# Performance work log

Measured on AMD Instinct MI355X. Metric: run time of the kernel, lower is better.

Reference implementation:

```python
import jax, jax.numpy as jnp
import numpy as np

D_MODEL = 1024
HEAD_SIZE = 64
BLOCK_SIZE = 2048
B, T = 4, 2048


def setup_inputs() -> dict:
    key = jax.random.key(0)
    ks = jax.random.split(key, 7)
    s = 1.0 / np.sqrt(D_MODEL)
    x = jax.random.normal(ks[0], (B, T, D_MODEL), dtype=jnp.float32)
    Wq = jax.random.uniform(ks[1], (D_MODEL, HEAD_SIZE), jnp.float32, -s, s)
    bq = jax.random.uniform(ks[2], (HEAD_SIZE,), jnp.float32, -s, s)
    Wk = jax.random.uniform(ks[3], (D_MODEL, HEAD_SIZE), jnp.float32, -s, s)
    bk = jax.random.uniform(ks[4], (HEAD_SIZE,), jnp.float32, -s, s)
    Wv = jax.random.uniform(ks[5], (D_MODEL, HEAD_SIZE), jnp.float32, -s, s)
    return {"x": x, "Wq": Wq, "bq": bq, "Wk": Wk, "bk": bk, "Wv": Wv, "mask": 1}


def reference(x, Wq, bq, Wk, bk, Wv, mask):
    # x: [B, T, C]; single attention head, dropout is identity (eval/p=0)
    Tlen = x.shape[1]
    q = x @ Wq + bq              # [B, T, hs]
    k = x @ Wk + bk              # [B, T, hs]
    v = x @ Wv                   # [B, T, hs] (no bias)
    hs = k.shape[-1]
    # Faithful to source: weights = QK^T / hs**(-0.5)  ==  QK^T * sqrt(hs)
    w = jnp.einsum('btd,bsd->bts', q, k) * jnp.sqrt(jnp.asarray(hs, x.dtype))
    if mask:
        causal = jnp.tril(jnp.ones((Tlen, Tlen), dtype=bool))
        w = jnp.where(causal, w, jnp.asarray(-jnp.inf, w.dtype))
    w = jax.nn.softmax(w, axis=-1)
    out = jnp.einsum('bts,bsd->btd', w, v)  # [B, T, hs]
    return out
```

## Files before the change

### kernel.cpp

```cpp
#include <hip/hip_runtime.h>
#include <hip/hip_bf16.h>

#define D_MODEL 1024
#define HS 64
#define T_LEN 2048
#define JCH 256
#define NCH 8

typedef __attribute__((ext_vector_type(8))) short bf16x8;
typedef __attribute__((ext_vector_type(4))) float f32x4;

__device__ inline void split8(const float* v, int4& hi, int4& lo) {
    union { unsigned short u[8]; int4 v4; } uh, ul;
    #pragma unroll
    for (int i = 0; i < 8; ++i) {
        const unsigned int b = __float_as_uint(v[i]);
        const unsigned short h = (unsigned short)(b >> 16);
        const float r = v[i] - __uint_as_float((unsigned int)h << 16);
        uh.u[i] = h;
        ul.u[i] = (unsigned short)(__float_as_uint(r) >> 16);
    }
    hi = uh.v4; lo = ul.v4;
}

__device__ inline unsigned short f2bf_rne(float f) {
    const unsigned int b = __float_as_uint(f);
    return (unsigned short)((b + 0x7FFFu + ((b >> 16) & 1u)) >> 16);
}
__device__ inline float bf2f(unsigned short h) {
    return __uint_as_float((unsigned int)h << 16);
}

__device__ inline void async_copy16(const short* g, short* l) {
    __builtin_amdgcn_global_load_lds(
        (const __attribute__((address_space(1))) void*)g,
        (__attribute__((address_space(3))) void*)l, 16, 0, 0);
}

__global__ __launch_bounds__(256) void prep_kernel(
    const float* __restrict__ Wq, const float* __restrict__ Wk,
    const float* __restrict__ Wv,
    short* __restrict__ wh, short* __restrict__ wl)
{
    __shared__ float tile[64][69];
    const int tid = threadIdx.x;
    const int wb  = blockIdx.x;
    const int kb  = wb & 15;
    const int m   = wb >> 4;
    const float* W = (m == 0) ? Wq : (m == 1) ? Wk : Wv;
    #pragma unroll
    for (int it = 0; it < 4; ++it) {
        const int idx = tid + 256 * it;
        const int kr = idx >> 4, c4 = idx & 15;
        *(float4*)&tile[kr][4 * c4] =
            *(const float4*)(W + (size_t)(kb * 64 + kr) * HS + 4 * c4);
    }
    __syncthreads();
    #pragma unroll
    for (int i = 0; i < 2; ++i) {
        const int s    = tid + 256 * i;
        const int ntl  = s >> 7;
        const int kcl  = (s >> 6) & 1;
        const int lane = s & 63;
        const int n    = ntl * 16 + (lane & 15);
        const int krel = kcl * 32 + (lane >> 4) * 8;
        float v[8];
        #pragma unroll
        for (int e = 0; e < 8; ++e) v[e] = tile[krel + e][n];
        int4 hi, lo;
        split8(v, hi, lo);
        const size_t off =
            ((size_t)((m * 4 + ntl) * 32 + kb * 2 + kcl) * 64 + lane) * 8;
        *(int4*)(wh + off) = hi;
        *(int4*)(wl + off) = lo;
    }
}

__device__ inline void stage_B(const short* __restrict__ wh,
                               const short* __restrict__ wl,
                               short* Bdst, int ch, int wave, int lane) {
    #pragma unroll
    for (int ii = 0; ii < 12; ++ii) {
        const int g   = wave * 12 + ii;
        const int nt  = g >> 2;
        const int kcl = (g >> 1) & 1;
        const int p   = g & 1;
        const short* src = (p ? wl : wh)
                         + ((size_t)(nt * 32 + ch * 2 + kcl)) * 512;
        async_copy16(src + lane * 8, Bdst + g * 512);
    }
}

__global__ __launch_bounds__(256) void qkv_kernel(
    const float* __restrict__ x,
    const short* __restrict__ wh, const short* __restrict__ wl,
    const float* __restrict__ bq, const float* __restrict__ bk,
    short* __restrict__ qfh, short* __restrict__ qfl,
    short* __restrict__ kfh, short* __restrict__ kfl, short* __restrict__ vf)
{
    __shared__ __align__(16) short A_lds[2][8 * 512];
    __shared__ __align__(16) short B_lds[2][48 * 512];

    const int tid   = threadIdx.x;
    const int r0    = blockIdx.x * 32;
    const int wave  = tid >> 6;
    const int lane  = tid & 63;
    const int mt_l  = tid >> 7;
    const int kcl_l = (tid >> 6) & 1;
    const int nt0   = wave * 3;

    const float* xrow = x + (size_t)(r0 + mt_l * 16 + (lane & 15)) * D_MODEL
                          + kcl_l * 32 + (lane >> 4) * 8;

    f32x4 acc[2][3];
    #pragma unroll
    for (int mt = 0; mt < 2; ++mt)
        #pragma unroll
        for (int j = 0; j < 3; ++j) acc[mt][j] = (f32x4)(0.f);

    {
        stage_B(wh, wl, &B_lds[0][0], 0, wave, lane);
        float v[8];
        *(float4*)&v[0] = *(const float4*)(xrow);
        *(float4*)&v[4] = *(const float4*)(xrow + 4);
        int4 hi, lo;
        split8(v, hi, lo);
        *(int4*)&A_lds[0][(mt_l * 4 + kcl_l * 2 + 0) * 512 + lane * 8] = hi;
        *(int4*)&A_lds[0][(mt_l * 4 + kcl_l * 2 + 1) * 512 + lane * 8] = lo;
    }
    __syncthreads();

    int cur = 0;
    for (int t = 0; t < 16; ++t) {
        float v[8];
        const bool pf = (t < 15);
        if (pf) {
            *(float4*)&v[0] = *(const float4*)(xrow + (t + 1) * 64);
            *(float4*)&v[4] = *(const float4*)(xrow + (t + 1) * 64 + 4);
            stage_B(wh, wl, &B_lds[cur ^ 1][0], t + 1, wave, lane);
        }
        #pragma unroll
        for (int kcl = 0; kcl < 2; ++kcl) {
            const bf16x8 a0h = *(const bf16x8*)&A_lds[cur][(0 + kcl * 2 + 0) * 512 + lane * 8];
            const bf16x8 a0l = *(const bf16x8*)&A_lds[cur][(0 + kcl * 2 + 1) * 512 + lane * 8];
            const bf16x8 a1h = *(const bf16x8*)&A_lds[cur][(4 + kcl * 2 + 0) * 512 + lane * 8];
            const bf16x8 a1l = *(const bf16x8*)&A_lds[cur][(4 + kcl * 2 + 1) * 512 + lane * 8];
            #pragma unroll
            for (int j = 0; j < 3; ++j) {
                const int gb = (nt0 + j) * 4 + kcl * 2;
                const bf16x8 bh = *(const bf16x8*)&B_lds[cur][(gb + 0) * 512 + lane * 8];
                const bf16x8 bl = *(const bf16x8*)&B_lds[cur][(gb + 1) * 512 + lane * 8];
                acc[0][j] = __builtin_amdgcn_mfma_f32_16x16x32_bf16(a0h, bh, acc[0][j], 0, 0, 0);
                acc[0][j] = __builtin_amdgcn_mfma_f32_16x16x32_bf16(a0h, bl, acc[0][j], 0, 0, 0);
                acc[0][j] = __builtin_amdgcn_mfma_f32_16x16x32_bf16(a0l, bh, acc[0][j], 0, 0, 0);
                acc[1][j] = __builtin_amdgcn_mfma_f32_16x16x32_bf16(a1h, bh, acc[1][j], 0, 0, 0);
                acc[1][j] = __builtin_amdgcn_mfma_f32_16x16x32_bf16(a1h, bl, acc[1][j], 0, 0, 0);
                acc[1][j] = __builtin_amdgcn_mfma_f32_16x16x32_bf16(a1l, bh, acc[1][j], 0, 0, 0);
            }
        }
        if (pf) {
            int4 hi, lo;
            split8(v, hi, lo);
            *(int4*)&A_lds[cur ^ 1][(mt_l * 4 + kcl_l * 2 + 0) * 512 + lane * 8] = hi;
            *(int4*)&A_lds[cur ^ 1][(mt_l * 4 + kcl_l * 2 + 1) * 512 + lane * 8] = lo;
        }
        __syncthreads();
        cur ^= 1;
    }

    const int quad = lane >> 4;
    const int l15  = lane & 15;
    #pragma unroll
    for (int mt = 0; mt < 2; ++mt) {
        const int rowb = r0 + mt * 16 + quad * 4;
        #pragma unroll
        for (int j = 0; j < 3; ++j) {
            const f32x4 a = acc[mt][j];
            const int c = (nt0 + j) * 16 + l15;
            if (c < 128) {
                const int cc    = (c < 64) ? c : (c - 64);
                const float bias = (c < 64) ? bq[cc] : bk[cc];
                short* dsth = (c < 64) ? qfh : kfh;
                short* dstl = (c < 64) ? qfl : kfl;
                const int tile16 = rowb >> 4;
                const int kc2   = cc >> 5;
                const int quadd = (cc & 31) >> 3;
                const int e     = cc & 7;
                #pragma unroll
                for (int r = 0; r < 4; ++r) {
                    const float val = a[r] + bias;
                    const unsigned int b = __float_as_uint(val);
                    const unsigned short h = (unsigned short)(b >> 16);
                    const float res = val - __uint_as_float((unsigned int)h << 16);
                    const unsigned short l16 = (unsigned short)(__float_as_uint(res) >> 16);
                    const int laned = ((rowb + r) & 15) | (quadd << 4);
                    const size_t off = ((size_t)((tile16 * 2 + kc2) * 64 + laned)) * 8 + e;
                    dsth[off] = (short)h;
                    dstl[off] = (short)l16;
                }
            } else {
                const int cv    = c - 128;
                const int vb    = rowb >> 6;
                const int jc2   = (rowb & 63) >> 5;
                const int quadd = (rowb & 31) >> 3;
                const int gg    = jc2 * 4 + (cv >> 4);
                const int laned = (cv & 15) | (quadd << 4);
                const size_t base = ((size_t)((vb * 8 + gg) * 64 + laned)) * 8 + (rowb & 7);
                short4 pk;
                pk.x = (short)f2bf_rne(a[0]);
                pk.y = (short)f2bf_rne(a[1]);
                pk.z = (short)f2bf_rne(a[2]);
                pk.w = (short)f2bf_rne(a[3]);
                *(short4*)(vf + base) = pk;
            }
        }
    }
}

__global__ __launch_bounds__(256) void attn_kernel(
    const short* __restrict__ qfh, const short* __restrict__ qfl,
    const short* __restrict__ kfh, const short* __restrict__ kfl,
    const short* __restrict__ vf, const int* __restrict__ maskp,
    float* __restrict__ part_O, float* __restrict__ part_ml, int BT)
{
    __shared__ __align__(16) short Kh[4096], Kl[4096];
    __shared__ __align__(16) short Vt[4096];
    __shared__ __align__(16) short Pl[4][16 * 72];

    const int tile  = blockIdx.x;
    const int chunk = blockIdx.y;
    const int r0 = tile * 64;
    const int tb = r0 / T_LEN;
    const int t0 = r0 - tb * T_LEN;
    const int mask = (*maskp != 0);
    const int n_max = mask ? (t0 + 64) : T_LEN;
    const int j0 = chunk * JCH;
    if (j0 >= n_max) return;
    const int hi_j = min(j0 + JCH, n_max);
    const int njt = (hi_j - j0 + 63) >> 6;

    const int tid  = threadIdx.x;
    const int w    = tid >> 6;
    const int lane = tid & 63;
    const int quad = lane >> 4;
    const int l15  = lane & 15;
    const int rw0  = t0 + 16 * w;
    const int rowa = r0 + 16 * w + quad * 4;

    bf16x8 qh[2], ql[2];
    {
        const size_t qt = (size_t)(r0 >> 4) + w;
        #pragma unroll
        for (int kc = 0; kc < 2; ++kc) {
            qh[kc] = *(const bf16x8*)&qfh[((qt * 2 + kc) * 64 + lane) * 8];
            ql[kc] = *(const bf16x8*)&qfl[((qt * 2 + kc) * 64 + lane) * 8];
        }
    }

    f32x4 oacc[4];
    #pragma unroll
    for (int nt = 0; nt < 4; ++nt) oacc[nt] = (f32x4)(0.f);
    float m_r[4] = {-INFINITY, -INFINITY, -INFINITY, -INFINITY};
    float l_r[4] = {0.f, 0.f, 0.f, 0.f};

    for (int jt = 0; jt < njt; ++jt) {
        const int jbase = j0 + jt * 64;
        __syncthreads();
        {
            const size_t kt0 = (size_t)(tb * 128) + (jbase >> 4);
            const size_t vb  = (size_t)(tb * 32) + (jbase >> 6);
            #pragma unroll
            for (int ii = 0; ii < 6; ++ii) {
                const int g = w * 6 + ii;
                if (g < 8) {
                    const short* src = kfh + ((kt0 + (g >> 1)) * 2 + (g & 1)) * 512;
                    async_copy16(src + lane * 8, &Kh[g * 512]);
                } else if (g < 16) {
                    const int gg = g - 8;
                    const short* src = kfl + ((kt0 + (gg >> 1)) * 2 + (gg & 1)) * 512;
                    async_copy16(src + lane * 8, &Kl[gg * 512]);
                } else {
                    const int gg = g - 16;
                    const short* src = vf + (vb * 8 + gg) * 512;
                    async_copy16(src + lane * 8, &Vt[gg * 512]);
                }
            }
        }
        __syncthreads();

        const bool active = (!mask) || (jbase <= rw0 + 15);
        if (active) {
            f32x4 sacc[4];
            #pragma unroll
            for (int jsub = 0; jsub < 4; ++jsub) {
                f32x4 s = (f32x4)(0.f);
                #pragma unroll
                for (int kc = 0; kc < 2; ++kc) {
                    const bf16x8 kh = *(const bf16x8*)&Kh[((jsub * 2 + kc) * 64 + lane) * 8];
                    const bf16x8 kl = *(const bf16x8*)&Kl[((jsub * 2 + kc) * 64 + lane) * 8];
                    s = __builtin_amdgcn_mfma_f32_16x16x32_bf16(qh[kc], kh, s, 0, 0, 0);
                    s = __builtin_amdgcn_mfma_f32_16x16x32_bf16(qh[kc], kl, s, 0, 0, 0);
                    s = __builtin_amdgcn_mfma_f32_16x16x32_bf16(ql[kc], kh, s, 0, 0, 0);
                }
                sacc[jsub] = s;
            }
            float sval[4][4], rmax[4];
            #pragma unroll
            for (int r = 0; r < 4; ++r) rmax[r] = -INFINITY;
            #pragma unroll
            for (int jsub = 0; jsub < 4; ++jsub) {
                const int jg = jbase + jsub * 16 + l15;
                #pragma unroll
                for (int r = 0; r < 4; ++r) {
                    const int tg = rw0 + quad * 4 + r;
                    const float vv = (mask && (jg > tg)) ? -INFINITY : 8.0f * sacc[jsub][r];
                    sval[jsub][r] = vv;
                    rmax[r] = fmaxf(rmax[r], vv);
                }
            }
            #pragma unroll
            for (int d = 1; d < 16; d <<= 1)
                #pragma unroll
                for (int r = 0; r < 4; ++r)
                    rmax[r] = fmaxf(rmax[r], __shfl_xor(rmax[r], d));
            float alpha[4], msafe[4];
            #pragma unroll
            for (int r = 0; r < 4; ++r) {
                const float mn = fmaxf(m_r[r], rmax[r]);
                msafe[r] = (mn == -INFINITY) ? 0.f : mn;
                alpha[r] = __expf(m_r[r] - msafe[r]);
                m_r[r] = mn;
            }
            short* Pw = &Pl[w][0];
            float rsum[4] = {0.f, 0.f, 0.f, 0.f};
            #pragma unroll
            for (int jsub = 0; jsub < 4; ++jsub) {
                #pragma unroll
                for (int r = 0; r < 4; ++r) {
                    const float e = __expf(sval[jsub][r] - msafe[r]);
                    const unsigned short eb = f2bf_rne(e);
                    Pw[(quad * 4 + r) * 72 + jsub * 16 + l15] = (short)eb;
                    rsum[r] += bf2f(eb);
                }
            }
            #pragma unroll
            for (int d = 1; d < 16; d <<= 1)
                #pragma unroll
                for (int r = 0; r < 4; ++r)
                    rsum[r] += __shfl_xor(rsum[r], d);
            #pragma unroll
            for (int r = 0; r < 4; ++r)
                l_r[r] = l_r[r] * alpha[r] + rsum[r];
            #pragma unroll
            for (int nt = 0; nt < 4; ++nt)
                #pragma unroll
                for (int r = 0; r < 4; ++r)
                    oacc[nt][r] *= alpha[r];
            bf16x8 pf[2];
            #pragma unroll
            for (int jc = 0; jc < 2; ++jc)
                pf[jc] = *(const bf16x8*)&Pw[l15 * 72 + jc * 32 + quad * 8];
            #pragma unroll
            for (int nt = 0; nt < 4; ++nt) {
                #pragma unroll
                for (int jc = 0; jc < 2; ++jc) {
                    const bf16x8 vfr = *(const bf16x8*)&Vt[((jc * 4 + nt) * 64 + lane) * 8];
                    oacc[nt] = __builtin_amdgcn_mfma_f32_16x16x32_bf16(pf[jc], vfr, oacc[nt], 0, 0, 0);
                }
            }
        }
    }

    #pragma unroll
    for (int nt = 0; nt < 4; ++nt)
        #pragma unroll
        for (int r = 0; r < 4; ++r)
            part_O[((size_t)(rowa + r) * NCH + chunk) * HS + nt * 16 + l15] = oacc[nt][r];
    if (l15 == 0) {
        #pragma unroll
        for (int r = 0; r < 4; ++r) {
            float2 ml;
            ml.x = m_r[r];
            ml.y = l_r[r];
            *(float2*)(part_ml + ((size_t)(rowa + r) * NCH + chunk) * 2) = ml;
        }
    }
}

__global__ __launch_bounds__(256) void combine_kernel(
    const float* __restrict__ part_O, const float* __restrict__ part_ml,
    const int* __restrict__ maskp, float* __restrict__ out)
{
    const int f = blockIdx.x * 256 + threadIdx.x;
    const int row = f >> 4;
    const int d4 = (f & 15) * 4;
    const int t = row & (T_LEN - 1);
    const int mask = (*maskp != 0);
    const int n = mask ? (t + 1) : T_LEN;
    const int nc = (n + JCH - 1) / JCH;

    const float2* mlp = (const float2*)(part_ml + (size_t)row * NCH * 2);
    float M = -INFINITY;
    for (int c = 0; c < nc; ++c) M = fmaxf(M, mlp[c].x);
    float L = 0.f;
    float Ox = 0.f, Oy = 0.f, Oz = 0.f, Ow = 0.f;
    for (int c = 0; c < nc; ++c) {
        const float2 ml = mlp[c];
        const float w = __expf(ml.x - M);
        L += ml.y * w;
        const float4 p = *(const float4*)(part_O + ((size_t)row * NCH + c) * HS + d4);
        Ox = fmaf(p.x, w, Ox);
        Oy = fmaf(p.y, w, Oy);
        Oz = fmaf(p.z, w, Oz);
        Ow = fmaf(p.w, w, Ow);
    }
    float4 res;
    res.x = Ox / L;
    res.y = Oy / L;
    res.z = Oz / L;
    res.w = Ow / L;
    *(float4*)(out + (size_t)row * HS + d4) = res;
}

extern "C" void kernel_launch(void* const* d_in, const int* in_sizes, int n_in,
                              void* d_out, int out_size, void* d_ws, size_t ws_size,
                              hipStream_t stream) {
    const float* x  = (const float*)d_in[0];
    const float* Wq = (const float*)d_in[1];
    const float* bq = (const float*)d_in[2];
    const float* Wk = (const float*)d_in[3];
    const float* bk = (const float*)d_in[4];
    const float* Wv = (const float*)d_in[5];
    const int* maskp = (const int*)d_in[6];

    const int BT = in_sizes[0] / D_MODEL;

    float* pO  = (float*)d_ws;
    float* pml = pO + (size_t)BT * NCH * HS;
    short* wh  = (short*)(pml + (size_t)BT * NCH * 2);
    short* wl  = wh + (size_t)192 * D_MODEL;
    short* qfh = wl + (size_t)192 * D_MODEL;
    short* qfl = qfh + (size_t)BT * HS;
    short* kfh = qfl + (size_t)BT * HS;
    short* kfl = kfh + (size_t)BT * HS;
    short* vf  = kfl + (size_t)BT * HS;

    prep_kernel<<<48, 256, 0, stream>>>(Wq, Wk, Wv, wh, wl);
    qkv_kernel<<<BT / 32, 256, 0, stream>>>(x, wh, wl, bq, bk,
                                            qfh, qfl, kfh, kfl, vf);
    dim3 agrid(BT / 64, NCH);
    attn_kernel<<<agrid, 256, 0, stream>>>(qfh, qfl, kfh, kfl, vf, maskp,
                                           pO, pml, BT);
    combine_kernel<<<(BT * 16) / 256, 256, 0, stream>>>(pO, pml, maskp, (float*)d_out);
}
```

Baseline: 138.8 us.

## Fuse four kernels into one persistent kernel with grid barriers

Replaces the prep, QKV projection, attention and combine launches with a single persistent kernel of 256 blocks that loops over work items in each phase. Phases are separated by a software grid barrier built on an atomic counter. The aim is to remove per-launch overhead and the idle tails between kernels. In exchange it relies on all 256 blocks being co-resident, which a 112KB shared buffer and one block per CU make plausible. It also caps parallelism in each phase at 256 blocks and adds barrier spin cost.

```diff
diff --git a/kernel.cpp b/kernel.cpp
--- a/kernel.cpp
+++ b/kernel.cpp
@@ -6,6 +6,7 @@
 #define T_LEN 2048
 #define JCH 256
 #define NCH 8
+#define NBLK 256
 
 typedef __attribute__((ext_vector_type(8))) short bf16x8;
 typedef __attribute__((ext_vector_type(4))) float f32x4;
@@ -35,45 +36,6 @@
     __builtin_amdgcn_global_load_lds(
         (const __attribute__((address_space(1))) void*)g,
         (__attribute__((address_space(3))) void*)l, 16, 0, 0);
-}
-
-__global__ __launch_bounds__(256) void prep_kernel(
-    const float* __restrict__ Wq, const float* __restrict__ Wk,
-    const float* __restrict__ Wv,
-    short* __restrict__ wh, short* __restrict__ wl)
-{
-    __shared__ float tile[64][69];
-    const int tid = threadIdx.x;
-    const int wb  = blockIdx.x;
-    const int kb  = wb & 15;
-    const int m   = wb >> 4;
-    const float* W = (m == 0) ? Wq : (m == 1) ? Wk : Wv;
-    #pragma unroll
-    for (int it = 0; it < 4; ++it) {
-        const int idx = tid + 256 * it;
-        const int kr = idx >> 4, c4 = idx & 15;
-        *(float4*)&tile[kr][4 * c4] =
-            *(const float4*)(W + (size_t)(kb * 64 + kr) * HS + 4 * c4);
-    }
-    __syncthreads();
-    #pragma unroll
-    for (int i = 0; i < 2; ++i) {
-        const int s    = tid + 256 * i;
-        const int ntl  = s >> 7;
-        const int kcl  = (s >> 6) & 1;
-        const int lane = s & 63;
-        const int n    = ntl * 16 + (lane & 15);
-        const int krel = kcl * 32 + (lane >> 4) * 8;
-        float v[8];
-        #pragma unroll
-        for (int e = 0; e < 8; ++e) v[e] = tile[krel + e][n];
-        int4 hi, lo;
-        split8(v, hi, lo);
-        const size_t off =
-            ((size_t)((m * 4 + ntl) * 32 + kb * 2 + kcl) * 64 + lane) * 8;
-        *(int4*)(wh + off) = hi;
-        *(int4*)(wl + off) = lo;
-    }
 }
 
 __device__ inline void stage_B(const short* __restrict__ wh,
@@ -91,335 +53,399 @@
     }
 }
 
-__global__ __launch_bounds__(256) void qkv_kernel(
+__device__ unsigned int g_tick;
+
+__device__ __forceinline__ void grid_barrier() {
+    __syncthreads();
+    __threadfence();
+    if (threadIdx.x == 0) {
+        const unsigned int t = __hip_atomic_fetch_add(
+            &g_tick, 1u, __ATOMIC_ACQ_REL, __HIP_MEMORY_SCOPE_AGENT);
+        const unsigned int target = ((t >> 8) + 1u) << 8;
+        while (__hip_atomic_load(&g_tick, __ATOMIC_ACQUIRE,
+                                 __HIP_MEMORY_SCOPE_AGENT) < target) {
+            __builtin_amdgcn_s_sleep(2);
+        }
+    }
+    __syncthreads();
+    __threadfence();
+}
+
+__global__ __launch_bounds__(256, 1) void fused_kernel(
     const float* __restrict__ x,
-    const short* __restrict__ wh, const short* __restrict__ wl,
+    const float* __restrict__ Wq, const float* __restrict__ Wk,
+    const float* __restrict__ Wv,
     const float* __restrict__ bq, const float* __restrict__ bk,
+    const int* __restrict__ maskp,
+    short* __restrict__ wh, short* __restrict__ wl,
     short* __restrict__ qfh, short* __restrict__ qfl,
-    short* __restrict__ kfh, short* __restrict__ kfl, short* __restrict__ vf)
+    short* __restrict__ kfh, short* __restrict__ kfl, short* __restrict__ vf,
+    float* __restrict__ part_O, float* __restrict__ part_ml,
+    float* __restrict__ out, int BT)
 {
-    __shared__ __align__(16) short A_lds[2][8 * 512];
-    __shared__ __align__(16) short B_lds[2][48 * 512];
-
-    const int tid   = threadIdx.x;
-    const int r0    = blockIdx.x * 32;
-    const int wave  = tid >> 6;
-    const int lane  = tid & 63;
-    const int mt_l  = tid >> 7;
-    const int kcl_l = (tid >> 6) & 1;
-    const int nt0   = wave * 3;
-
-    const float* xrow = x + (size_t)(r0 + mt_l * 16 + (lane & 15)) * D_MODEL
-                          + kcl_l * 32 + (lane >> 4) * 8;
-
-    f32x4 acc[2][3];
-    #pragma unroll
-    for (int mt = 0; mt < 2; ++mt)
+    __shared__ __align__(16) char smem[114688];
+    const int tid = threadIdx.x;
+    const int bx  = blockIdx.x;
+
+    if (bx < 48) {
+        float (*tile)[69] = (float (*)[69])smem;
+        const int kb = bx & 15;
+        const int m  = bx >> 4;
+        const float* W = (m == 0) ? Wq : (m == 1) ? Wk : Wv;
         #pragma unroll
-        for (int j = 0; j < 3; ++j) acc[mt][j] = (f32x4)(0.f);
-
-    {
-        stage_B(wh, wl, &B_lds[0][0], 0, wave, lane);
-        float v[8];
-        *(float4*)&v[0] = *(const float4*)(xrow);
-        *(float4*)&v[4] = *(const float4*)(xrow + 4);
-        int4 hi, lo;
-        split8(v, hi, lo);
-        *(int4*)&A_lds[0][(mt_l * 4 + kcl_l * 2 + 0) * 512 + lane * 8] = hi;
-        *(int4*)&A_lds[0][(mt_l * 4 + kcl_l * 2 + 1) * 512 + lane * 8] = lo;
-    }
-    __syncthreads();
-
-    int cur = 0;
-    for (int t = 0; t < 16; ++t) {
-        float v[8];
-        const bool pf = (t < 15);
-        if (pf) {
-            *(float4*)&v[0] = *(const float4*)(xrow + (t + 1) * 64);
-            *(float4*)&v[4] = *(const float4*)(xrow + (t + 1) * 64 + 4);
-            stage_B(wh, wl, &B_lds[cur ^ 1][0], t + 1, wave, lane);
-        }
+        for (int it = 0; it < 4; ++it) {
+            const int idx = tid + 256 * it;
+            const int kr = idx >> 4, c4 = idx & 15;
+            *(float4*)&tile[kr][4 * c4] =
+                *(const float4*)(W + (size_t)(kb * 64 + kr) * HS + 4 * c4);
+        }
+        __syncthreads();
         #pragma unroll
-        for (int kcl = 0; kcl < 2; ++kcl) {
-            const bf16x8 a0h = *(const bf16x8*)&A_lds[cur][(0 + kcl * 2 + 0) * 512 + lane * 8];
-            const bf16x8 a0l = *(const bf16x8*)&A_lds[cur][(0 + kcl * 2 + 1) * 512 + lane * 8];
-            const bf16x8 a1h = *(const bf16x8*)&A_lds[cur][(4 + kcl * 2 + 0) * 512 + lane * 8];
-            const bf16x8 a1l = *(const bf16x8*)&A_lds[cur][(4 + kcl * 2 + 1) * 512 + lane * 8];
-            #pragma unroll
-            for (int j = 0; j < 3; ++j) {
-                const int gb = (nt0 + j) * 4 + kcl * 2;
-                const bf16x8 bh = *(const bf16x8*)&B_lds[cur][(gb + 0) * 512 + lane * 8];
-                const bf16x8 bl = *(const bf16x8*)&B_lds[cur][(gb + 1) * 512 + lane * 8];
-                acc[0][j] = __builtin_amdgcn_mfma_f32_16x16x32_bf16(a0h, bh, acc[0][j], 0, 0, 0);
-                acc[0][j] = __builtin_amdgcn_mfma_f32_16x16x32_bf16(a0h, bl, acc[0][j], 0, 0, 0);
-                acc[0][j] = __builtin_amdgcn_mfma_f32_16x16x32_bf16(a0l, bh, acc[0][j], 0, 0, 0);
-                acc[1][j] = __builtin_amdgcn_mfma_f32_16x16x32_bf16(a1h, bh, acc[1][j], 0, 0, 0);
-                acc[1][j] = __builtin_amdgcn_mfma_f32_16x16x32_bf16(a1h, bl, acc[1][j], 0, 0, 0);
-                acc[1][j] = __builtin_amdgcn_mfma_f32_16x16x32_bf16(a1l, bh, acc[1][j], 0, 0, 0);
-            }
-        }
-        if (pf) {
+        for (int i = 0; i < 2; ++i) {
+            const int s    = tid + 256 * i;
+            const int ntl  = s >> 7;
+            const int kcl  = (s >> 6) & 1;
+            const int lane = s & 63;
+            const int n    = ntl * 16 + (lane & 15);
+            const int krel = kcl * 32 + (lane >> 4) * 8;
+            float v[8];
+            #pragma unroll
+            for (int e = 0; e < 8; ++e) v[e] = tile[krel + e][n];
             int4 hi, lo;
             split8(v, hi, lo);
-            *(int4*)&A_lds[cur ^ 1][(mt_l * 4 + kcl_l * 2 + 0) * 512 + lane * 8] = hi;
-            *(int4*)&A_lds[cur ^ 1][(mt_l * 4 + kcl_l * 2 + 1) * 512 + lane * 8] = lo;
+            const size_t off =
+                ((size_t)((m * 4 + ntl) * 32 + kb * 2 + kcl) * 64 + lane) * 8;
+            *(int4*)(wh + off) = hi;
+            *(int4*)(wl + off) = lo;
+        }
+    }
+    grid_barrier();
+
+    for (int g = bx; g < (BT >> 5); g += NBLK) {
+        short* const Abase = (short*)smem;
+        short* const Bbase = (short*)(smem + 16384);
+        const int r0    = g * 32;
+        const int wave  = tid >> 6;
+        const int lane  = tid & 63;
+        const int mt_l  = tid >> 7;
+        const int kcl_l = (tid >> 6) & 1;
+        const int nt0   = wave * 3;
+
+        const float* xrow = x + (size_t)(r0 + mt_l * 16 + (lane & 15)) * D_MODEL
+                              + kcl_l * 32 + (lane >> 4) * 8;
+
+        f32x4 acc[2][3];
+        #pragma unroll
+        for (int mt = 0; mt < 2; ++mt)
+            #pragma unroll
+            for (int j = 0; j < 3; ++j) acc[mt][j] = (f32x4)(0.f);
+
+        {
+            stage_B(wh, wl, Bbase, 0, wave, lane);
+            float v[8];
+            *(float4*)&v[0] = *(const float4*)(xrow);
+            *(float4*)&v[4] = *(const float4*)(xrow + 4);
+            int4 hi, lo;
+            split8(v, hi, lo);
+            *(int4*)&Abase[(mt_l * 4 + kcl_l * 2 + 0) * 512 + lane * 8] = hi;
+            *(int4*)&Abase[(mt_l * 4 + kcl_l * 2 + 1) * 512 + lane * 8] = lo;
         }
         __syncthreads();
-        cur ^= 1;
-    }
-
-    const int quad = lane >> 4;
-    const int l15  = lane & 15;
-    #pragma unroll
-    for (int mt = 0; mt < 2; ++mt) {
-        const int rowb = r0 + mt * 16 + quad * 4;
+
+        int cur = 0;
+        for (int t = 0; t < 16; ++t) {
+            float v[8];
+            const bool pf = (t < 15);
+            if (pf) {
+                *(float4*)&v[0] = *(const float4*)(xrow + (t + 1) * 64);
+                *(float4*)&v[4] = *(const float4*)(xrow + (t + 1) * 64 + 4);
+                stage_B(wh, wl, Bbase + (cur ^ 1) * 24576, t + 1, wave, lane);
+            }
+            const short* Ac = Abase + cur * 4096;
+            const short* Bc = Bbase + cur * 24576;
+            #pragma unroll
+            for (int kcl = 0; kcl < 2; ++kcl) {
+                const bf16x8 a0h = *(const bf16x8*)&Ac[(0 + kcl * 2 + 0) * 512 + lane * 8];
+                const bf16x8 a0l = *(const bf16x8*)&Ac[(0 + kcl * 2 + 1) * 512 + lane * 8];
+                const bf16x8 a1h = *(const bf16x8*)&Ac[(4 + kcl * 2 + 0) * 512 + lane * 8];
+                const bf16x8 a1l = *(const bf16x8*)&Ac[(4 + kcl * 2 + 1) * 512 + lane * 8];
+                #pragma unroll
+                for (int j = 0; j < 3; ++j) {
+                    const int gb = (nt0 + j) * 4 + kcl * 2;
+                    const bf16x8 bh = *(const bf16x8*)&Bc[(gb + 0) * 512 + lane * 8];
+                    const bf16x8 bl = *(const bf16x8*)&Bc[(gb + 1) * 512 + lane * 8];
+                    acc[0][j] = __builtin_amdgcn_mfma_f32_16x16x32_bf16(a0h, bh, acc[0][j], 0, 0, 0);
+                    acc[0][j] = __builtin_amdgcn_mfma_f32_16x16x32_bf16(a0h, bl, acc[0][j], 0, 0, 0);
+                    acc[0][j] = __builtin_amdgcn_mfma_f32_16x16x32_bf16(a0l, bh, acc[0][j], 0, 0, 0);
+                    acc[1][j] = __builtin_amdgcn_mfma_f32_16x16x32_bf16(a1h, bh, acc[1][j], 0, 0, 0);
+                    acc[1][j] = __builtin_amdgcn_mfma_f32_16x16x32_bf16(a1h, bl, acc[1][j], 0, 0, 0);
+                    acc[1][j] = __builtin_amdgcn_mfma_f32_16x16x32_bf16(a1l, bh, acc[1][j], 0, 0, 0);
+                }
+            }
+            if (pf) {
+                int4 hi, lo;
+                split8(v, hi, lo);
+                short* An = Abase + (cur ^ 1) * 4096;
+                *(int4*)&An[(mt_l * 4 + kcl_l * 2 + 0) * 512 + lane * 8] = hi;
+                *(int4*)&An[(mt_l * 4 + kcl_l * 2 + 1) * 512 + lane * 8] = lo;
+            }
+            __syncthreads();
+            cur ^= 1;
+        }
+
+        const int quad = lane >> 4;
+        const int l15  = lane & 15;
         #pragma unroll
-        for (int j = 0; j < 3; ++j) {
-            const f32x4 a = acc[mt][j];
-            const int c = (nt0 + j) * 16 + l15;
-            if (c < 128) {
-                const int cc    = (c < 64) ? c : (c - 64);
-                const float bias = (c < 64) ? bq[cc] : bk[cc];
-                short* dsth = (c < 64) ? qfh : kfh;
-                short* dstl = (c < 64) ? qfl : kfl;
-                const int tile16 = rowb >> 4;
-                const int kc2   = cc >> 5;
-                const int quadd = (cc & 31) >> 3;
-                const int e     = cc & 7;
-                #pragma unroll
-                for (int r = 0; r < 4; ++r) {
-                    const float val = a[r] + bias;
-                    const unsigned int b = __float_as_uint(val);
-                    const unsigned short h = (unsigned short)(b >> 16);
-                    const float res = val - __uint_as_float((unsigned int)h << 16);
-                    const unsigned short l16 = (unsigned short)(__float_as_uint(res) >> 16);
-                    const int laned = ((rowb + r) & 15) | (quadd << 4);
-                    const size_t off = ((size_t)((tile16 * 2 + kc2) * 64 + laned)) * 8 + e;
-                    dsth[off] = (short)h;
-                    dstl[off] = (short)l16;
-                }
-            } else {
-                const int cv    = c - 128;
-                const int vb    = rowb >> 6;
-                const int jc2   = (rowb & 63) >> 5;
-                const int quadd = (rowb & 31) >> 3;
-                const int gg    = jc2 * 4 + (cv >> 4);
-                const int laned = (cv & 15) | (quadd << 4);
-                const size_t base = ((size_t)((vb * 8 + gg) * 64 + laned)) * 8 + (rowb & 7);
-                short4 pk;
-                pk.x = (short)f2bf_rne(a[0]);
-                pk.y = (short)f2bf_rne(a[1]);
-                pk.z = (short)f2bf_rne(a[2]);
-                pk.w = (short)f2bf_rne(a[3]);
-                *(short4*)(vf + base) = pk;
-            }
-        }
-    }
-}
-
-__global__ __launch_bounds__(256) void attn_kernel(
-    const short* __restrict__ qfh, const short* __restrict__ qfl,
-    const short* __restrict__ kfh, const short* __restrict__ kfl,
-    const short* __restrict__ vf, const int* __restrict__ maskp,
-    float* __restrict__ part_O, float* __restrict__ part_ml, int BT)
-{
-    __shared__ __align__(16) short Kh[4096], Kl[4096];
-    __shared__ __align__(16) short Vt[4096];
-    __shared__ __align__(16) short Pl[4][16 * 72];
-
-    const int tile  = blockIdx.x;
-    const int chunk = blockIdx.y;
-    const int r0 = tile * 64;
-    const int tb = r0 / T_LEN;
-    const int t0 = r0 - tb * T_LEN;
-    const int mask = (*maskp != 0);
-    const int n_max = mask ? (t0 + 64) : T_LEN;
-    const int j0 = chunk * JCH;
-    if (j0 >= n_max) return;
-    const int hi_j = min(j0 + JCH, n_max);
-    const int njt = (hi_j - j0 + 63) >> 6;
-
-    const int tid  = threadIdx.x;
-    const int w    = tid >> 6;
-    const int lane = tid & 63;
-    const int quad = lane >> 4;
-    const int l15  = lane & 15;
-    const int rw0  = t0 + 16 * w;
-    const int rowa = r0 + 16 * w + quad * 4;
-
-    bf16x8 qh[2], ql[2];
+        for (int mt = 0; mt < 2; ++mt) {
+            const int rowb = r0 + mt * 16 + quad * 4;
+            #pragma unroll
+            for (int j = 0; j < 3; ++j) {
+                const f32x4 a = acc[mt][j];
+                const int c = (nt0 + j) * 16 + l15;
+                if (c < 128) {
+                    const int cc    = (c < 64) ? c : (c - 64);
+                    const float bias = (c < 64) ? bq[cc] : bk[cc];
+                    short* dsth = (c < 64) ? qfh : kfh;
+                    short* dstl = (c < 64) ? qfl : kfl;
+                    const int tile16 = rowb >> 4;
+                    const int kc2   = cc >> 5;
+                    const int quadd = (cc & 31) >> 3;
+                    const int e     = cc & 7;
+                    #pragma unroll
+                    for (int r = 0; r < 4; ++r) {
+                        const float val = a[r] + bias;
+                        const unsigned int b = __float_as_uint(val);
+                        const unsigned short h = (unsigned short)(b >> 16);
+                        const float res = val - __uint_as_float((unsigned int)h << 16);
+                        const unsigned short l16 = (unsigned short)(__float_as_uint(res) >> 16);
+                        const int laned = ((rowb + r) & 15) | (quadd << 4);
+                        const size_t off = ((size_t)((tile16 * 2 + kc2) * 64 + laned)) * 8 + e;
+                        dsth[off] = (short)h;
+                        dstl[off] = (short)l16;
+                    }
+                } else {
+                    const int cv    = c - 128;
+                    const int vb    = rowb >> 6;
+                    const int jc2   = (rowb & 63) >> 5;
+                    const int quadd = (rowb & 31) >> 3;
+                    const int gg    = jc2 * 4 + (cv >> 4);
+                    const int laned = (cv & 15) | (quadd << 4);
+                    const size_t base = ((size_t)((vb * 8 + gg) * 64 + laned)) * 8 + (rowb & 7);
+                    short4 pk;
+                    pk.x = (short)f2bf_rne(a[0]);
+                    pk.y = (short)f2bf_rne(a[1]);
+                    pk.z = (short)f2bf_rne(a[2]);
+                    pk.w = (short)f2bf_rne(a[3]);
+                    *(short4*)(vf + base) = pk;
+                }
+            }
+        }
+    }
+    grid_barrier();
+
     {
-        const size_t qt = (size_t)(r0 >> 4) + w;
-        #pragma unroll
-        for (int kc = 0; kc < 2; ++kc) {
-            qh[kc] = *(const bf16x8*)&qfh[((qt * 2 + kc) * 64 + lane) * 8];
-            ql[kc] = *(const bf16x8*)&qfl[((qt * 2 + kc) * 64 + lane) * 8];
-        }
-    }
-
-    f32x4 oacc[4];
-    #pragma unroll
-    for (int nt = 0; nt < 4; ++nt) oacc[nt] = (f32x4)(0.f);
-    float m_r[4] = {-INFINITY, -INFINITY, -INFINITY, -INFINITY};
-    float l_r[4] = {0.f, 0.f, 0.f, 0.f};
-
-    for (int jt = 0; jt < njt; ++jt) {
-        const int jbase = j0 + jt * 64;
-        __syncthreads();
-        {
-            const size_t kt0 = (size_t)(tb * 128) + (jbase >> 4);
-            const size_t vb  = (size_t)(tb * 32) + (jbase >> 6);
-            #pragma unroll
-            for (int ii = 0; ii < 6; ++ii) {
-                const int g = w * 6 + ii;
-                if (g < 8) {
-                    const short* src = kfh + ((kt0 + (g >> 1)) * 2 + (g & 1)) * 512;
-                    async_copy16(src + lane * 8, &Kh[g * 512]);
-                } else if (g < 16) {
-                    const int gg = g - 8;
-                    const short* src = kfl + ((kt0 + (gg >> 1)) * 2 + (gg & 1)) * 512;
-                    async_copy16(src + lane * 8, &Kl[gg * 512]);
-                } else {
-                    const int gg = g - 16;
-                    const short* src = vf + (vb * 8 + gg) * 512;
-                    async_copy16(src + lane * 8, &Vt[gg * 512]);
-                }
-            }
-        }
-        __syncthreads();
-
-        const bool active = (!mask) || (jbase <= rw0 + 15);
-        if (active) {
-            f32x4 sacc[4];
-            #pragma unroll
-            for (int jsub = 0; jsub < 4; ++jsub) {
-                f32x4 s = (f32x4)(0.f);
+        const int ntile  = BT >> 6;
+        const int nitems = ntile * NCH;
+        short* const Kh = (short*)smem;
+        short* const Kl = Kh + 4096;
+        short* const Vt = Kh + 8192;
+        short* const Pm = Kh + 12288;
+
+        const int w    = tid >> 6;
+        const int lane = tid & 63;
+        const int quad = lane >> 4;
+        const int l15  = lane & 15;
+        const int mask = (*maskp != 0);
+
+        for (int itm = bx; itm < nitems; itm += NBLK) {
+            const int tl    = itm % ntile;
+            const int chunk = itm / ntile;
+            const int r0 = tl * 64;
+            const int tb = r0 / T_LEN;
+            const int t0 = r0 - tb * T_LEN;
+            const int n_max = mask ? (t0 + 64) : T_LEN;
+            const int j0 = chunk * JCH;
+            if (j0 >= n_max) continue;
+            const int hi_j = min(j0 + JCH, n_max);
+            const int njt = (hi_j - j0 + 63) >> 6;
+
+            const int rw0  = t0 + 16 * w;
+            const int rowa = r0 + 16 * w + quad * 4;
+
+            bf16x8 qh[2], ql[2];
+            {
+                const size_t qt = (size_t)(r0 >> 4) + w;
                 #pragma unroll
                 for (int kc = 0; kc < 2; ++kc) {
-                    const bf16x8 kh = *(const bf16x8*)&Kh[((jsub * 2 + kc) * 64 + lane) * 8];
-                    const bf16x8 kl = *(const bf16x8*)&Kl[((jsub * 2 + kc) * 64 + lane) * 8];
-                    s = __builtin_amdgcn_mfma_f32_16x16x32_bf16(qh[kc], kh, s, 0, 0, 0);
-                    s = __builtin_amdgcn_mfma_f32_16x16x32_bf16(qh[kc], kl, s, 0, 0, 0);
-                    s = __builtin_amdgcn_mfma_f32_16x16x32_bf16(ql[kc], kh, s, 0, 0, 0);
-                }
-                sacc[jsub] = s;
-            }
-            float sval[4][4], rmax[4];
-            #pragma unroll
-            for (int r = 0; r < 4; ++r) rmax[r] = -INFINITY;
-            #pragma unroll
-            for (int jsub = 0; jsub < 4; ++jsub) {
-                const int jg = jbase + jsub * 16 + l15;
-                #pragma unroll
-                for (int r = 0; r < 4; ++r) {
-                    const int tg = rw0 + quad * 4 + r;
-                    const float vv = (mask && (jg > tg)) ? -INFINITY : 8.0f * sacc[jsub][r];
-                    sval[jsub][r] = vv;
-                    rmax[r] = fmaxf(rmax[r], vv);
-                }
-            }
-            #pragma unroll
-            for (int d = 1; d < 16; d <<= 1)
-                #pragma unroll
-                for (int r = 0; r < 4; ++r)
-                    rmax[r] = fmaxf(rmax[r], __shfl_xor(rmax[r], d));
-            float alpha[4], msafe[4];
-            #pragma unroll
-            for (int r = 0; r < 4; ++r) {
-                const float mn = fmaxf(m_r[r], rmax[r]);
-                msafe[r] = (mn == -INFINITY) ? 0.f : mn;
-                alpha[r] = __expf(m_r[r] - msafe[r]);
-                m_r[r] = mn;
-            }
-            short* Pw = &Pl[w][0];
-            float rsum[4] = {0.f, 0.f, 0.f, 0.f};
-            #pragma unroll
-            for (int jsub = 0; jsub < 4; ++jsub) {
-                #pragma unroll
-                for (int r = 0; r < 4; ++r) {
-                    const float e = __expf(sval[jsub][r] - msafe[r]);
-                    const unsigned short eb = f2bf_rne(e);
-                    Pw[(quad * 4 + r) * 72 + jsub * 16 + l15] = (short)eb;
-                    rsum[r] += bf2f(eb);
-                }
-            }
-            #pragma unroll
-            for (int d = 1; d < 16; d <<= 1)
-                #pragma unroll
-                for (int r = 0; r < 4; ++r)
-                    rsum[r] += __shfl_xor(rsum[r], d);
-            #pragma unroll
-            for (int r = 0; r < 4; ++r)
-                l_r[r] = l_r[r] * alpha[r] + rsum[r];
+                    qh[kc] = *(const bf16x8*)&qfh[((qt * 2 + kc) * 64 + lane) * 8];
+                    ql[kc] = *(const bf16x8*)&qfl[((qt * 2 + kc) * 64 + lane) * 8];
+                }
+            }
+
+            f32x4 oacc[4];
+            #pragma unroll
+            for (int nt = 0; nt < 4; ++nt) oacc[nt] = (f32x4)(0.f);
+            float m_r[4] = {-INFINITY, -INFINITY, -INFINITY, -INFINITY};
+            float l_r[4] = {0.f, 0.f, 0.f, 0.f};
+
+            for (int jt = 0; jt < njt; ++jt) {
+                const int jbase = j0 + jt * 64;
+                __syncthreads();
+                {
+                    const size_t kt0 = (size_t)(tb * 128) + (jbase >> 4);
+                    const size_t vb  = (size_t)(tb * 32) + (jbase >> 6);
+                    #pragma unroll
+                    for (int ii = 0; ii < 6; ++ii) {
+                        const int g = w * 6 + ii;
+                        if (g < 8) {
+                            const short* src = kfh + ((kt0 + (g >> 1)) * 2 + (g & 1)) * 512;
+                            async_copy16(src + lane * 8, &Kh[g * 512]);
+                        } else if (g < 16) {
+                            const int gg = g - 8;
+                            const short* src = kfl + ((kt0 + (gg >> 1)) * 2 + (gg & 1)) * 512;
+                            async_copy16(src + lane * 8, &Kl[gg * 512]);
+                        } else {
+                            const int gg = g - 16;
+                            const short* src = vf + (vb * 8 + gg) * 512;
+                            async_copy16(src + lane * 8, &Vt[gg * 512]);
+                        }
+                    }
+                }
+                __syncthreads();
+
+                const bool active = (!mask) || (jbase <= rw0 + 15);
+                if (active) {
+                    f32x4 sacc[4];
+                    #pragma unroll
+                    for (int jsub = 0; jsub < 4; ++jsub) {
+                        f32x4 s = (f32x4)(0.f);
+                        #pragma unroll
+                        for (int kc = 0; kc < 2; ++kc) {
+                            const bf16x8 kh = *(const bf16x8*)&Kh[((jsub * 2 + kc) * 64 + lane) * 8];
+                            const bf16x8 kl = *(const bf16x8*)&Kl[((jsub * 2 + kc) * 64 + lane) * 8];
+                            s = __builtin_amdgcn_mfma_f32_16x16x32_bf16(qh[kc], kh, s, 0, 0, 0);
+                            s = __builtin_amdgcn_mfma_f32_16x16x32_bf16(qh[kc], kl, s, 0, 0, 0);
+                            s = __builtin_amdgcn_mfma_f32_16x16x32_bf16(ql[kc], kh, s, 0, 0, 0);
+                        }
+                        sacc[jsub] = s;
+                    }
+                    float sval[4][4], rmax[4];
+                    #pragma unroll
+                    for (int r = 0; r < 4; ++r) rmax[r] = -INFINITY;
+                    #pragma unroll
+                    for (int jsub = 0; jsub < 4; ++jsub) {
+                        const int jg = jbase + jsub * 16 + l15;
+                        #pragma unroll
+                        for (int r = 0; r < 4; ++r) {
+                            const int tg = rw0 + quad * 4 + r;
+                            const float vv = (mask && (jg > tg)) ? -INFINITY : 8.0f * sacc[jsub][r];
+                            sval[jsub][r] = vv;
+                            rmax[r] = fmaxf(rmax[r], vv);
+                        }
+                    }
+                    #pragma unroll
+                    for (int d = 1; d < 16; d <<= 1)
+                        #pragma unroll
+                        for (int r = 0; r < 4; ++r)
+                            rmax[r] = fmaxf(rmax[r], __shfl_xor(rmax[r], d));
+                    float alpha[4], msafe[4];
+                    #pragma unroll
+                    for (int r = 0; r < 4; ++r) {
+                        const float mn = fmaxf(m_r[r], rmax[r]);
+                        msafe[r] = (mn == -INFINITY) ? 0.f : mn;
+                        alpha[r] = __expf(m_r[r] - msafe[r]);
+                        m_r[r] = mn;
+                    }
+                    short* Pw = Pm + w * 1152;
+                    float rsum[4] = {0.f, 0.f, 0.f, 0.f};
+                    #pragma unroll
+                    for (int jsub = 0; jsub < 4; ++jsub) {
+                        #pragma unroll
+                        for (int r = 0; r < 4; ++r) {
+                            const float e = __expf(sval[jsub][r] - msafe[r]);
+                            const unsigned short eb = f2bf_rne(e);
+                            Pw[(quad * 4 + r) * 72 + jsub * 16 + l15] = (short)eb;
+                            rsum[r] += bf2f(eb);
+                        }
+                    }
+                    #pragma unroll
+                    for (int d = 1; d < 16; d <<= 1)
+                        #pragma unroll
+                        for (int r = 0; r < 4; ++r)
+                            rsum[r] += __shfl_xor(rsum[r], d);
+                    #pragma unroll
+                    for (int r = 0; r < 4; ++r)
+                        l_r[r] = l_r[r] * alpha[r] + rsum[r];
+                    #pragma unroll
+                    for (int nt = 0; nt < 4; ++nt)
+                        #pragma unroll
+                        for (int r = 0; r < 4; ++r)
+                            oacc[nt][r] *= alpha[r];
+                    bf16x8 pf[2];
+                    #pragma unroll
+                    for (int jc = 0; jc < 2; ++jc)
+                        pf[jc] = *(const bf16x8*)&Pw[l15 * 72 + jc * 32 + quad * 8];
+                    #pragma unroll
+                    for (int nt = 0; nt < 4; ++nt) {
+                        #pragma unroll
+                        for (int jc = 0; jc < 2; ++jc) {
+                            const bf16x8 vfr = *(const bf16x8*)&Vt[((jc * 4 + nt) * 64 + lane) * 8];
+                            oacc[nt] = __builtin_amdgcn_mfma_f32_16x16x32_bf16(pf[jc], vfr, oacc[nt], 0, 0, 0);
+                        }
+                    }
+                }
+            }
+
             #pragma unroll
             for (int nt = 0; nt < 4; ++nt)
                 #pragma unroll
                 for (int r = 0; r < 4; ++r)
-                    oacc[nt][r] *= alpha[r];
-            bf16x8 pf[2];
-            #pragma unroll
-            for (int jc = 0; jc < 2; ++jc)
-                pf[jc] = *(const bf16x8*)&Pw[l15 * 72 + jc * 32 + quad * 8];
-            #pragma unroll
-            for (int nt = 0; nt < 4; ++nt) {
+                    part_O[((size_t)(rowa + r) * NCH + chunk) * HS + nt * 16 + l15] = oacc[nt][r];
+            if (l15 == 0) {
                 #pragma unroll
-                for (int jc = 0; jc < 2; ++jc) {
-                    const bf16x8 vfr = *(const bf16x8*)&Vt[((jc * 4 + nt) * 64 + lane) * 8];
-                    oacc[nt] = __builtin_amdgcn_mfma_f32_16x16x32_bf16(pf[jc], vfr, oacc[nt], 0, 0, 0);
-                }
-            }
-        }
-    }
-
-    #pragma unroll
-    for (int nt = 0; nt < 4; ++nt)
-        #pragma unroll
-        for (int r = 0; r < 4; ++r)
-            part_O[((size_t)(rowa + r) * NCH + chunk) * HS + nt * 16 + l15] = oacc[nt][r];
-    if (l15 == 0) {
-        #pragma unroll
-        for (int r = 0; r < 4; ++r) {
-            float2 ml;
-            ml.x = m_r[r];
-            ml.y = l_r[r];
-            *(float2*)(part_ml + ((size_t)(rowa + r) * NCH + chunk) * 2) = ml;
-        }
-    }
-}
-
-__global__ __launch_bounds__(256) void combine_kernel(
-    const float* __restrict__ part_O, const float* __restrict__ part_ml,
-    const int* __restrict__ maskp, float* __restrict__ out)
-{
-    const int f = blockIdx.x * 256 + threadIdx.x;
-    const int row = f >> 4;
-    const int d4 = (f & 15) * 4;
-    const int t = row & (T_LEN - 1);
-    const int mask = (*maskp != 0);
-    const int n = mask ? (t + 1) : T_LEN;
-    const int nc = (n + JCH - 1) / JCH;
-
-    const float2* mlp = (const float2*)(part_ml + (size_t)row * NCH * 2);
-    float M = -INFINITY;
-    for (int c = 0; c < nc; ++c) M = fmaxf(M, mlp[c].x);
-    float L = 0.f;
-    float Ox = 0.f, Oy = 0.f, Oz = 0.f, Ow = 0.f;
-    for (int c = 0; c < nc; ++c) {
-        const float2 ml = mlp[c];
-        const float w = __expf(ml.x - M);
-        L += ml.y * w;
-        const float4 p = *(const float4*)(part_O + ((size_t)row * NCH + c) * HS + d4);
-        Ox = fmaf(p.x, w, Ox);
-        Oy = fmaf(p.y, w, Oy);
-        Oz = fmaf(p.z, w, Oz);
-        Ow = fmaf(p.w, w, Ow);
-    }
-    float4 res;
-    res.x = Ox / L;
-    res.y = Oy / L;
-    res.z = Oz / L;
-    res.w = Ow / L;
-    *(float4*)(out + (size_t)row * HS + d4) = res;
+                for (int r = 0; r < 4; ++r) {
+                    float2 ml;
+                    ml.x = m_r[r];
+                    ml.y = l_r[r];
+                    *(float2*)(part_ml + ((size_t)(rowa + r) * NCH + chunk) * 2) = ml;
+                }
+            }
+        }
+    }
+    grid_barrier();
+
+    {
+        const int mask = (*maskp != 0);
+        for (int f = bx * 256 + tid; f < BT * 16; f += NBLK * 256) {
+            const int row = f >> 4;
+            const int d4 = (f & 15) * 4;
+            const int t = row & (T_LEN - 1);
+            const int n = mask ? (t + 1) : T_LEN;
+            const int nc = (n + JCH - 1) / JCH;
+
+            const float2* mlp = (const float2*)(part_ml + (size_t)row * NCH * 2);
+            float M = -INFINITY;
+            for (int c = 0; c < nc; ++c) M = fmaxf(M, mlp[c].x);
+            float L = 0.f;
+            float Ox = 0.f, Oy = 0.f, Oz = 0.f, Ow = 0.f;
+            for (int c = 0; c < nc; ++c) {
+                const float2 ml = mlp[c];
+                const float wgt = __expf(ml.x - M);
+                L += ml.y * wgt;
+                const float4 p = *(const float4*)(part_O + ((size_t)row * NCH + c) * HS + d4);
+                Ox = fmaf(p.x, wgt, Ox);
+                Oy = fmaf(p.y, wgt, Oy);
+                Oz = fmaf(p.z, wgt, Oz);
+                Ow = fmaf(p.w, wgt, Ow);
+            }
+            float4 res;
+            res.x = Ox / L;
+            res.y = Oy / L;
+            res.z = Oz / L;
+            res.w = Ow / L;
+            *(float4*)(out + (size_t)row * HS + d4) = res;
+        }
+    }
 }
 
 extern "C" void kernel_launch(void* const* d_in, const int* in_sizes, int n_in,
@@ -445,11 +471,8 @@
     short* kfl = kfh + (size_t)BT * HS;
     short* vf  = kfl + (size_t)BT * HS;
 
-    prep_kernel<<<48, 256, 0, stream>>>(Wq, Wk, Wv, wh, wl);
-    qkv_kernel<<<BT / 32, 256, 0, stream>>>(x, wh, wl, bq, bk,
-                                            qfh, qfl, kfh, kfl, vf);
-    dim3 agrid(BT / 64, NCH);
-    attn_kernel<<<agrid, 256, 0, stream>>>(qfh, qfl, kfh, kfl, vf, maskp,
-                                           pO, pml, BT);
-    combine_kernel<<<(BT * 16) / 256, 256, 0, stream>>>(pO, pml, maskp, (float*)d_out);
-}
+    fused_kernel<<<NBLK, 256, 0, stream>>>(
+        x, Wq, Wk, Wv, bq, bk, maskp,
+        wh, wl, qfh, qfl, kfh, kfl, vf,
+        pO, pml, (float*)d_out, BT);
+}
```

Result: slower. 358.7 us (+158.4%).

## Double QKV projection row tile to 64 and use explicit waitcnt barriers

Applied to the files above, without the earlier changes.

The QKV projection block now covers 64 rows instead of 32, so each wave computes four M-tiles and reuses every staged B (weight) tile across twice as many MFMAs. This halves how often the shared weight chunks are reloaded from global memory into LDS. __syncthreads is replaced by explicit vmcnt/lgkmcnt waits, s_barrier and sched_barrier so the weight prefetch can stay in flight while the current chunk is computed. In exchange the kernel uses more LDS, more accumulator registers and half as many blocks, which lowers parallelism on a large GPU.

```diff
diff --git a/kernel.cpp b/kernel.cpp
--- a/kernel.cpp
+++ b/kernel.cpp
@@ -91,6 +91,9 @@
     }
 }
 
+#define WAITVM(N) asm volatile("s_waitcnt vmcnt(" #N ")" ::: "memory")
+#define WAITLGKM0 asm volatile("s_waitcnt lgkmcnt(0)" ::: "memory")
+
 __global__ __launch_bounds__(256) void qkv_kernel(
     const float* __restrict__ x,
     const short* __restrict__ wh, const short* __restrict__ wl,
@@ -98,80 +101,108 @@
     short* __restrict__ qfh, short* __restrict__ qfl,
     short* __restrict__ kfh, short* __restrict__ kfl, short* __restrict__ vf)
 {
-    __shared__ __align__(16) short A_lds[2][8 * 512];
+    __shared__ __align__(16) short A_lds[2][16 * 512];
     __shared__ __align__(16) short B_lds[2][48 * 512];
 
     const int tid   = threadIdx.x;
-    const int r0    = blockIdx.x * 32;
+    const int r0    = blockIdx.x * 64;
     const int wave  = tid >> 6;
     const int lane  = tid & 63;
-    const int mt_l  = tid >> 7;
-    const int kcl_l = (tid >> 6) & 1;
     const int nt0   = wave * 3;
 
-    const float* xrow = x + (size_t)(r0 + mt_l * 16 + (lane & 15)) * D_MODEL
-                          + kcl_l * 32 + (lane >> 4) * 8;
-
-    f32x4 acc[2][3];
-    #pragma unroll
-    for (int mt = 0; mt < 2; ++mt)
+    const int fp   = tid >> 5;
+    const int l1   = tid & 31;
+    const int mt_c = fp >> 1;
+    const int kcl_c = fp & 1;
+    const float* xp = x + (size_t)(r0 + mt_c * 16 + (l1 & 15)) * D_MODEL
+                        + kcl_c * 32 + (l1 >> 4) * 8;
+
+    f32x4 acc[4][3];
+    #pragma unroll
+    for (int mt = 0; mt < 4; ++mt)
         #pragma unroll
         for (int j = 0; j < 3; ++j) acc[mt][j] = (f32x4)(0.f);
 
     {
+        float v1[8], v2[8];
+        *(float4*)&v1[0] = *(const float4*)(xp);
+        *(float4*)&v1[4] = *(const float4*)(xp + 4);
+        *(float4*)&v2[0] = *(const float4*)(xp + 16);
+        *(float4*)&v2[4] = *(const float4*)(xp + 20);
         stage_B(wh, wl, &B_lds[0][0], 0, wave, lane);
-        float v[8];
-        *(float4*)&v[0] = *(const float4*)(xrow);
-        *(float4*)&v[4] = *(const float4*)(xrow + 4);
         int4 hi, lo;
-        split8(v, hi, lo);
-        *(int4*)&A_lds[0][(mt_l * 4 + kcl_l * 2 + 0) * 512 + lane * 8] = hi;
-        *(int4*)&A_lds[0][(mt_l * 4 + kcl_l * 2 + 1) * 512 + lane * 8] = lo;
-    }
-    __syncthreads();
+        split8(v1, hi, lo);
+        *(int4*)&A_lds[0][(fp * 2 + 0) * 512 + l1 * 8] = hi;
+        *(int4*)&A_lds[0][(fp * 2 + 1) * 512 + l1 * 8] = lo;
+        split8(v2, hi, lo);
+        *(int4*)&A_lds[0][(fp * 2 + 0) * 512 + (l1 + 32) * 8] = hi;
+        *(int4*)&A_lds[0][(fp * 2 + 1) * 512 + (l1 + 32) * 8] = lo;
+        WAITLGKM0;
+        __builtin_amdgcn_s_barrier();
+        __builtin_amdgcn_sched_barrier(0);
+    }
 
     int cur = 0;
     for (int t = 0; t < 16; ++t) {
-        float v[8];
+        float v1[8], v2[8];
         const bool pf = (t < 15);
         if (pf) {
-            *(float4*)&v[0] = *(const float4*)(xrow + (t + 1) * 64);
-            *(float4*)&v[4] = *(const float4*)(xrow + (t + 1) * 64 + 4);
+            const float* xn = xp + (t + 1) * 64;
+            *(float4*)&v1[0] = *(const float4*)(xn);
+            *(float4*)&v1[4] = *(const float4*)(xn + 4);
+            *(float4*)&v2[0] = *(const float4*)(xn + 16);
+            *(float4*)&v2[4] = *(const float4*)(xn + 20);
             stage_B(wh, wl, &B_lds[cur ^ 1][0], t + 1, wave, lane);
-        }
+            WAITVM(16);
+        } else {
+            WAITVM(0);
+        }
+        __builtin_amdgcn_sched_barrier(0);
+
+        const short* Ac = &A_lds[cur][0];
+        const short* Bc = &B_lds[cur][0];
         #pragma unroll
         for (int kcl = 0; kcl < 2; ++kcl) {
-            const bf16x8 a0h = *(const bf16x8*)&A_lds[cur][(0 + kcl * 2 + 0) * 512 + lane * 8];
-            const bf16x8 a0l = *(const bf16x8*)&A_lds[cur][(0 + kcl * 2 + 1) * 512 + lane * 8];
-            const bf16x8 a1h = *(const bf16x8*)&A_lds[cur][(4 + kcl * 2 + 0) * 512 + lane * 8];
-            const bf16x8 a1l = *(const bf16x8*)&A_lds[cur][(4 + kcl * 2 + 1) * 512 + lane * 8];
+            bf16x8 ah[4], al[4];
+            #pragma unroll
+            for (int mt = 0; mt < 4; ++mt) {
+                ah[mt] = *(const bf16x8*)&Ac[((mt * 2 + kcl) * 2 + 0) * 512 + lane * 8];
+                al[mt] = *(const bf16x8*)&Ac[((mt * 2 + kcl) * 2 + 1) * 512 + lane * 8];
+            }
             #pragma unroll
             for (int j = 0; j < 3; ++j) {
                 const int gb = (nt0 + j) * 4 + kcl * 2;
-                const bf16x8 bh = *(const bf16x8*)&B_lds[cur][(gb + 0) * 512 + lane * 8];
-                const bf16x8 bl = *(const bf16x8*)&B_lds[cur][(gb + 1) * 512 + lane * 8];
-                acc[0][j] = __builtin_amdgcn_mfma_f32_16x16x32_bf16(a0h, bh, acc[0][j], 0, 0, 0);
-                acc[0][j] = __builtin_amdgcn_mfma_f32_16x16x32_bf16(a0h, bl, acc[0][j], 0, 0, 0);
-                acc[0][j] = __builtin_amdgcn_mfma_f32_16x16x32_bf16(a0l, bh, acc[0][j], 0, 0, 0);
-                acc[1][j] = __builtin_amdgcn_mfma_f32_16x16x32_bf16(a1h, bh, acc[1][j], 0, 0, 0);
-                acc[1][j] = __builtin_amdgcn_mfma_f32_16x16x32_bf16(a1h, bl, acc[1][j], 0, 0, 0);
-                acc[1][j] = __builtin_amdgcn_mfma_f32_16x16x32_bf16(a1l, bh, acc[1][j], 0, 0, 0);
-            }
-        }
+                const bf16x8 bh = *(const bf16x8*)&Bc[(gb + 0) * 512 + lane * 8];
+                const bf16x8 bl = *(const bf16x8*)&Bc[(gb + 1) * 512 + lane * 8];
+                #pragma unroll
+                for (int mt = 0; mt < 4; ++mt) {
+                    acc[mt][j] = __builtin_amdgcn_mfma_f32_16x16x32_bf16(ah[mt], bh, acc[mt][j], 0, 0, 0);
+                    acc[mt][j] = __builtin_amdgcn_mfma_f32_16x16x32_bf16(ah[mt], bl, acc[mt][j], 0, 0, 0);
+                    acc[mt][j] = __builtin_amdgcn_mfma_f32_16x16x32_bf16(al[mt], bh, acc[mt][j], 0, 0, 0);
+                }
+            }
+        }
+
         if (pf) {
+            short* An = &A_lds[cur ^ 1][0];
             int4 hi, lo;
-            split8(v, hi, lo);
-            *(int4*)&A_lds[cur ^ 1][(mt_l * 4 + kcl_l * 2 + 0) * 512 + lane * 8] = hi;
-            *(int4*)&A_lds[cur ^ 1][(mt_l * 4 + kcl_l * 2 + 1) * 512 + lane * 8] = lo;
-        }
-        __syncthreads();
+            split8(v1, hi, lo);
+            *(int4*)&An[(fp * 2 + 0) * 512 + l1 * 8] = hi;
+            *(int4*)&An[(fp * 2 + 1) * 512 + l1 * 8] = lo;
+            split8(v2, hi, lo);
+            *(int4*)&An[(fp * 2 + 0) * 512 + (l1 + 32) * 8] = hi;
+            *(int4*)&An[(fp * 2 + 1) * 512 + (l1 + 32) * 8] = lo;
+        }
+        WAITLGKM0;
+        __builtin_amdgcn_s_barrier();
+        __builtin_amdgcn_sched_barrier(0);
         cur ^= 1;
     }
 
     const int quad = lane >> 4;
     const int l15  = lane & 15;
     #pragma unroll
-    for (int mt = 0; mt < 2; ++mt) {
+    for (int mt = 0; mt < 4; ++mt) {
         const int rowb = r0 + mt * 16 + quad * 4;
         #pragma unroll
         for (int j = 0; j < 3; ++j) {
@@ -446,7 +477,7 @@
     short* vf  = kfl + (size_t)BT * HS;
 
     prep_kernel<<<48, 256, 0, stream>>>(Wq, Wk, Wv, wh, wl);
-    qkv_kernel<<<BT / 32, 256, 0, stream>>>(x, wh, wl, bq, bk,
+    qkv_kernel<<<BT / 64, 256, 0, stream>>>(x, wh, wl, bq, bk,
                                             qfh, qfl, kfh, kfl, vf);
     dim3 agrid(BT / 64, NCH);
     attn_kernel<<<agrid, 256, 0, stream>>>(qfh, qfl, kfh, kfl, vf, maskp,
```

Result: slower. 147.7 us (+6.4%).
